# Optimization experiments

Measured on AMD Instinct MI355X. Metric: run time of the kernel, lower is better.

Reference implementation:

```python
import jax, jax.numpy as jnp
import numpy as np

B, Q, C = 16, 2048, 256
SCORE_THRESH = 0.05   # lowered from 0.7 so the mask is non-trivial with 256 classes
NMS_THRESH = 0.7
LABEL_OFFSET = 1e5    # batched_nms trick: offset boxes per class so cross-class IoU ~ 0


def box_cxcywh_to_xyxy(b):
    cx, cy, w, h = jnp.split(b, 4, axis=-1)
    return jnp.concatenate([cx - 0.5 * w, cy - 0.5 * h, cx + 0.5 * w, cy + 0.5 * h], axis=-1)


def pairwise_iou(boxes):
    # boxes: [N,4] xyxy -> iou: [N,N]
    area = jnp.clip(boxes[:, 2] - boxes[:, 0], 0) * jnp.clip(boxes[:, 3] - boxes[:, 1], 0)
    lt = jnp.maximum(boxes[:, None, :2], boxes[None, :, :2])
    rb = jnp.minimum(boxes[:, None, 2:], boxes[None, :, 2:])
    wh = jnp.clip(rb - lt, 0)
    inter = wh[..., 0] * wh[..., 1]
    union = area[:, None] + area[None, :] - inter
    return inter / jnp.maximum(union, 1e-6)


def nms_single(boxes, scores, labels, valid):
    # Emulates torchvision batched_nms with fixed-size (padded) output:
    # returns score-sorted boxes/scores/labels plus a boolean keep mask.
    n = boxes.shape[0]
    boxes_off = boxes + labels.astype(boxes.dtype)[:, None] * LABEL_OFFSET
    order = jnp.argsort(jnp.where(valid, scores, -jnp.inf))[::-1]
    b_off = boxes_off[order]
    s = scores[order]
    l = labels[order]
    v = valid[order]
    iou = pairwise_iou(b_off)  # [N,N], class-offset so only same-class overlap
    idx = jnp.arange(n)

    def step(keep, x):
        row, i = x  # row: iou of box i vs all
        sup = (row > NMS_THRESH) & (idx > i) & keep[i]
        return keep & ~sup, None

    keep, _ = jax.lax.scan(step, v, (iou, idx))
    return boxes[order], s, l, keep & v


def setup_inputs() -> dict:
    key = jax.random.key(0)
    k1, k2, k3 = jax.random.split(key, 3)
    pred_logits = jax.random.normal(k1, (B, Q, C), dtype=jnp.float32)
    pred_boxes = jax.random.uniform(k2, (B, Q, 4), dtype=jnp.float32)
    target_sizes = jax.random.randint(k3, (B, 2), 480, 1333, dtype=jnp.int32)
    return {"pred_logits": pred_logits, "pred_boxes": pred_boxes, "target_sizes": target_sizes}


def reference(pred_logits, pred_boxes, target_sizes):
    prob = jax.nn.softmax(pred_logits, axis=-1)
    cls_prob = prob[..., :-1]            # drop 'no-object' class
    scores = cls_prob.max(axis=-1)       # [B,Q]
    labels = cls_prob.argmax(axis=-1)    # [B,Q]
    boxes = box_cxcywh_to_xyxy(pred_boxes)
    ts = target_sizes.astype(boxes.dtype)
    img_h, img_w = ts[:, 0], ts[:, 1]
    scale = jnp.stack([img_w, img_h, img_w, img_h], axis=1)  # [B,4]
    boxes = boxes * scale[:, None, :]
    valid = scores >= SCORE_THRESH
    out_boxes, out_scores, out_labels, keep = jax.vmap(nms_single)(boxes, scores, labels, valid)
    return out_boxes, out_scores, out_labels, keep
```

## Files before the change

### kernel.cpp

```cpp
#include <hip/hip_runtime.h>
#include <math.h>

#define NB 16
#define BQ 2048
#define NC 256
#define NL 255

typedef unsigned long long u64;
typedef unsigned int u32;
typedef unsigned short u16;
typedef unsigned char u8;

__device__ __forceinline__ u32 ord_f32(float f) {
  u32 b = __float_as_uint(f);
  return (b & 0x80000000u) ? ~b : (b | 0x80000000u);
}

__global__ __launch_bounds__(256) void score_box_kernel(
    const float* __restrict__ logits,
    const float* __restrict__ pboxes,
    const int* __restrict__ tsz,
    float* __restrict__ ws)
{
#pragma clang fp contract(off)
  const int lane = threadIdx.x & 63;
  const int g = lane & 15;
  const int wv = threadIdx.x >> 6;
  const int q = (blockIdx.x * 4 + wv) * 4 + (lane >> 4);
  const float* row = logits + (size_t)q * NC + g * 16;
  const float4 la = *reinterpret_cast<const float4*>(row);
  const float4 lb4 = *reinterpret_cast<const float4*>(row + 4);
  const float4 lc = *reinterpret_cast<const float4*>(row + 8);
  const float4 ld = *reinterpret_cast<const float4*>(row + 12);

  float m = fmaxf(fmaxf(fmaxf(la.x, la.y), fmaxf(la.z, la.w)),
           fmaxf(fmaxf(fmaxf(lb4.x, lb4.y), fmaxf(lb4.z, lb4.w)),
           fmaxf(fmaxf(fmaxf(lc.x, lc.y), fmaxf(lc.z, lc.w)),
                 fmaxf(fmaxf(ld.x, ld.y), fmaxf(ld.z, ld.w)))));
  #pragma unroll
  for (int d = 1; d < 16; d <<= 1) m = fmaxf(m, __shfl_xor(m, d));

  float4 ea, eb, ec, ed;
  ea.x = expf(la.x - m);  ea.y = expf(la.y - m);  ea.z = expf(la.z - m);  ea.w = expf(la.w - m);
  eb.x = expf(lb4.x - m); eb.y = expf(lb4.y - m); eb.z = expf(lb4.z - m); eb.w = expf(lb4.w - m);
  ec.x = expf(lc.x - m);  ec.y = expf(lc.y - m);  ec.z = expf(lc.z - m);  ec.w = expf(lc.w - m);
  ed.x = expf(ld.x - m);  ed.y = expf(ld.y - m);  ed.z = expf(ld.z - m);  ed.w = expf(ld.w - m);

  float s = (((ea.x + ea.y) + (ea.z + ea.w)) + ((eb.x + eb.y) + (eb.z + eb.w)))
          + (((ec.x + ec.y) + (ec.z + ec.w)) + ((ed.x + ed.y) + (ed.z + ed.w)));
  #pragma unroll
  for (int d = 1; d < 16; d <<= 1) s += __shfl_xor(s, d);

  const int c0 = g * 16;
  float bp = ea.x / s; int bc = c0;
  float p;
  p = ea.y / s; if (p > bp) { bp = p; bc = c0 + 1; }
  p = ea.z / s; if (p > bp) { bp = p; bc = c0 + 2; }
  p = ea.w / s; if (p > bp) { bp = p; bc = c0 + 3; }
  p = eb.x / s; if (p > bp) { bp = p; bc = c0 + 4; }
  p = eb.y / s; if (p > bp) { bp = p; bc = c0 + 5; }
  p = eb.z / s; if (p > bp) { bp = p; bc = c0 + 6; }
  p = eb.w / s; if (p > bp) { bp = p; bc = c0 + 7; }
  p = ec.x / s; if (p > bp) { bp = p; bc = c0 + 8; }
  p = ec.y / s; if (p > bp) { bp = p; bc = c0 + 9; }
  p = ec.z / s; if (p > bp) { bp = p; bc = c0 + 10; }
  p = ec.w / s; if (p > bp) { bp = p; bc = c0 + 11; }
  p = ed.x / s; if (p > bp) { bp = p; bc = c0 + 12; }
  p = ed.y / s; if (p > bp) { bp = p; bc = c0 + 13; }
  p = ed.z / s; if (p > bp) { bp = p; bc = c0 + 14; }
  p = ed.w / s; if (g != 15 && p > bp) { bp = p; bc = c0 + 15; }
  #pragma unroll
  for (int d = 1; d < 16; d <<= 1) {
    const float op = __shfl_xor(bp, d);
    const int   oc = __shfl_xor(bc, d);
    if (op > bp || (op == bp && oc < bc)) { bp = op; bc = oc; }
  }

  if (g == 0) {
    const int b = q >> 11;
    float hf = (float)tsz[b * 2 + 0];
    float wf = (float)tsz[b * 2 + 1];
    float4 pb = *reinterpret_cast<const float4*>(pboxes + (size_t)q * 4);
    float hw = 0.5f * pb.z, hh = 0.5f * pb.w;
    float4 ob;
    ob.x = (pb.x - hw) * wf;
    ob.y = (pb.y - hh) * hf;
    ob.z = (pb.x + hw) * wf;
    ob.w = (pb.y + hh) * hf;
    *reinterpret_cast<float4*>(ws + (size_t)q * 4) = ob;
    ws[NB * BQ * 4 + q] = bp;
    ws[NB * BQ * 5 + q] = (float)bc;
  }
}

__global__ __launch_bounds__(1024) void sort_nms_kernel(
    const float* __restrict__ ws, float* __restrict__ out)
{
#pragma clang fp contract(off)
  __shared__ __align__(16) u64 cvk[BQ];
  __shared__ u32 rnk[BQ];
  __shared__ u32 lgl[BQ];
  __shared__ float4 bxo[BQ];
  __shared__ u32 stg_g[BQ];
  __shared__ u16 gpos[BQ];
  __shared__ u8 grpk[BQ];
  __shared__ u32 offl[256];
  __shared__ u32 kcnt[256];
  __shared__ u32 wval[16], winv[16];

  const int b = blockIdx.x;
  const int tid = threadIdx.x;
  const int lane = tid & 63;
  const int wv = tid >> 6;
  const float* bws = ws + (size_t)b * BQ * 4;
  const float* sws = ws + NB * BQ * 4 + (size_t)b * BQ;
  const float* lws = ws + NB * BQ * 5 + (size_t)b * BQ;
  float* boxes_g  = out + (size_t)b * BQ * 4;
  float* scores_g = out + NB * BQ * 4 + (size_t)b * BQ;
  float* labels_g = out + NB * BQ * 5 + (size_t)b * BQ;
  float* keep_g   = out + NB * BQ * 6 + (size_t)b * BQ;

  const int q0 = 2 * tid;
  float2 s2 = *reinterpret_cast<const float2*>(sws + q0);
  float2 lf = *reinterpret_cast<const float2*>(lws + q0);
  float4 bb0 = *reinterpret_cast<const float4*>(bws + (size_t)q0 * 4);
  float4 bb1 = *reinterpret_cast<const float4*>(bws + (size_t)q0 * 4 + 4);
  const u32 l0 = (u32)(int)lf.x, l1 = (u32)(int)lf.y;
  rnk[tid] = 0; rnk[tid + 1024] = 0;
  lgl[tid] = 0; lgl[tid + 1024] = 0;
  if (tid < 256) kcnt[tid] = 0;
  const bool v0 = (s2.x >= 0.05f), v1 = (s2.y >= 0.05f);
  const u64 f0 = ((u64)ord_f32(s2.x) << 32) | ((u32)q0 << 8) | l0;
  const u64 f1 = ((u64)ord_f32(s2.y) << 32) | ((u32)(q0 + 1) << 8) | l1;
  const u64 b0 = __ballot(v0), b1 = __ballot(v1);
  if (lane == 0) {
    const u32 c = (u32)(__popcll(b0) + __popcll(b1));
    wval[wv] = c;
    winv[wv] = 128u - c;
  }
  __syncthreads();

  int nv = 0, voff = 0, ioff = 0;
  #pragma unroll
  for (int w = 0; w < 16; ++w) {
    const int c = (int)wval[w];
    nv += c;
    if (w < wv) { voff += c; ioff += (int)winv[w]; }
  }
  const int tinv = BQ - nv;
  const u64 below = (1ull << lane) - 1ull;
  const int vr0 = voff + (int)__popcll(b0 & below) + (int)__popcll(b1 & below);
  const int ir0 = ioff + (int)__popcll(~b0 & below) + (int)__popcll(~b1 & below);
  const int vr1 = vr0 + (v0 ? 1 : 0);
  const int ir1 = ir0 + (v0 ? 0 : 1);
  if (v0) cvk[vr0] = f0;
  else {
    const int ip = nv + (tinv - 1 - ir0);
    *reinterpret_cast<float4*>(boxes_g + (size_t)ip * 4) = bb0;
    scores_g[ip] = s2.x; labels_g[ip] = lf.x; keep_g[ip] = 0.0f;
  }
  if (v1) cvk[vr1] = f1;
  else {
    const int ip = nv + (tinv - 1 - ir1);
    *reinterpret_cast<float4*>(boxes_g + (size_t)ip * 4) = bb1;
    scores_g[ip] = s2.y; labels_g[ip] = lf.y; keep_g[ip] = 0.0f;
  }
  __syncthreads();

  const int nvc = (nv + 63) >> 6;
  {
    const int nitems = nvc * nvc;
    for (int it = wv; it < nitems; it += 16) {
      const int sc_ = it / nvc;
      const int jc = it - sc_ * nvc;
      const int slot = (sc_ << 6) + lane;
      const u64 ki = cvk[slot];
      const u32 li = (u32)ki & 255u;
      const int j0 = jc << 6;
      int lim = nv - j0; if (lim > 64) lim = 64;
      const u64* jp = &cvk[j0];
      u32 cgt = 0, lgt = 0, llt = 0;
      #pragma unroll 8
      for (int l = 0; l < lim; ++l) {
        const u64 kj = jp[l];
        const u32 lj = (u32)kj & 255u;
        const u32 gx = (kj > ki) ? 1u : 0u;
        cgt += gx;
        lgt += gx & ((lj == li) ? 1u : 0u);
        llt += (lj < li) ? 1u : 0u;
      }
      if (slot < nv) {
        if (cgt) atomicAdd(&rnk[slot], cgt);
        if (lgt | llt) atomicAdd(&lgl[slot], (lgt << 16) | llt);
      }
    }
  }
  __syncthreads();

  for (int slot = tid; slot < nv; slot += 1024) {
    const u64 ki = cvk[slot];
    const u32 p = rnk[slot];
    const u32 ll = lgl[slot];
    const u32 lgt = ll >> 16, llt = ll & 0xFFFFu;
    const u32 oi = (u32)(ki >> 8) & (BQ - 1);
    const u32 li = (u32)ki & 255u;
    const float4 A = *reinterpret_cast<const float4*>(bws + (size_t)oi * 4);
    *reinterpret_cast<float4*>(boxes_g + (size_t)p * 4) = A;
    scores_g[p] = __uint_as_float((u32)(ki >> 32) & 0x7FFFFFFFu);
    labels_g[p] = (float)li;
    const float lc = (float)li * 100000.0f;
    float4 Ao;
    Ao.x = A.x + lc; Ao.y = A.y + lc; Ao.z = A.z + lc; Ao.w = A.w + lc;
    bxo[p] = Ao;
    gpos[llt + lgt] = (u16)p;
    stg_g[p] = (llt << 16) | lgt;
    offl[li] = llt;
    atomicAdd(&kcnt[li], 1u);
  }
  __syncthreads();

  for (int p = tid; p < nv; p += 1024) {
    const u32 sg = stg_g[p];
    const u32 st = sg >> 16, g = sg & 0xFFFFu;
    if (g < 64) {
      const float4 Ao = bxo[p];
      const float areaA = fmaxf(Ao.z - Ao.x, 0.0f) * fmaxf(Ao.w - Ao.y, 0.0f);
      u64 m = 0;
      for (u32 r = 0; r < g; ++r) {
        const int p2 = gpos[st + r];
        const float4 Bo = bxo[p2];
        const float areaB = fmaxf(Bo.z - Bo.x, 0.0f) * fmaxf(Bo.w - Bo.y, 0.0f);
        const float ltx = fmaxf(Ao.x, Bo.x), lty = fmaxf(Ao.y, Bo.y);
        const float rbx = fminf(Ao.z, Bo.z), rby = fminf(Ao.w, Bo.w);
        const float iw = fmaxf(rbx - ltx, 0.0f), ih = fmaxf(rby - lty, 0.0f);
        const float inter = iw * ih;
        const float uni = (areaA + areaB) - inter;
        const float iou = inter / fmaxf(uni, 1e-6f);
        if (iou > 0.7f) m |= (1ull << r);
      }
      cvk[st + g] = m;
    }
  }
  __syncthreads();

  if (tid < NL) {
    const int k = (int)kcnt[tid];
    if (k > 0) {
      const int st = (int)offl[tid];
      if (k <= 64) {
        u64 kept = 0;
        for (int r = 0; r < k; ++r) {
          const u64 m = cvk[st + r];
          const int keep = ((m & kept) == 0) ? 1 : 0;
          kept |= (u64)keep << r;
          keep_g[gpos[st + r]] = keep ? 1.0f : 0.0f;
        }
      } else {
        for (int a = 0; a < k; ++a) {
          const int p = gpos[st + a];
          const float4 Ao = bxo[p];
          const float areaA = fmaxf(Ao.z - Ao.x, 0.0f) * fmaxf(Ao.w - Ao.y, 0.0f);
          int keep = 1;
          for (int e = 0; e < a; ++e) {
            if (!grpk[st + e]) continue;
            const int p2 = gpos[st + e];
            const float4 Bo = bxo[p2];
            const float areaB = fmaxf(Bo.z - Bo.x, 0.0f) * fmaxf(Bo.w - Bo.y, 0.0f);
            const float ltx = fmaxf(Ao.x, Bo.x), lty = fmaxf(Ao.y, Bo.y);
            const float rbx = fminf(Ao.z, Bo.z), rby = fminf(Ao.w, Bo.w);
            const float iw = fmaxf(rbx - ltx, 0.0f), ih = fmaxf(rby - lty, 0.0f);
            const float inter = iw * ih;
            const float uni = (areaA + areaB) - inter;
            const float iou = inter / fmaxf(uni, 1e-6f);
            if (iou > 0.7f) { keep = 0; break; }
          }
          grpk[st + a] = (u8)keep;
          keep_g[p] = keep ? 1.0f : 0.0f;
        }
      }
    }
  }
}

extern "C" void kernel_launch(void* const* d_in, const int* in_sizes, int n_in,
                              void* d_out, int out_size, void* d_ws, size_t ws_size,
                              hipStream_t stream) {
  const float* logits = (const float*)d_in[0];
  const float* pboxes = (const float*)d_in[1];
  const int*   tsz    = (const int*)d_in[2];
  float* out = (float*)d_out;
  float* ws  = (float*)d_ws;
  score_box_kernel<<<NB * BQ / 16, 256, 0, stream>>>(logits, pboxes, tsz, ws);
  sort_nms_kernel<<<NB, 1024, 0, stream>>>(ws, out);
}
```

Measured before the change: 36.85 us.

## Register-block rank counting, cache boxes in LDS, stage intermediates in output buffer

The all-pairs rank/label-count loop now gives each lane two query keys and reads the key array with 128-bit shared loads. The tail is padded with a sentinel key so the inner loop has a fixed trip count of 64 and no per-iteration bound check. Boxes are staged in shared memory so the scatter after ranking reads from LDS instead of global memory. The score kernel now writes its intermediates straight into the output buffer, which the sort kernel reads and then overwrites in place, so the separate workspace is no longer used. The cost is about 32 KB more LDS per block and a dependence on every read finishing before the first in-place write.

```diff
diff --git a/kernel.cpp b/kernel.cpp
--- a/kernel.cpp
+++ b/kernel.cpp
@@ -20,7 +20,7 @@
     const float* __restrict__ logits,
     const float* __restrict__ pboxes,
     const int* __restrict__ tsz,
-    float* __restrict__ ws)
+    float* __restrict__ out)
 {
 #pragma clang fp contract(off)
   const int lane = threadIdx.x & 63;
@@ -87,19 +87,19 @@
     ob.y = (pb.y - hh) * hf;
     ob.z = (pb.x + hw) * wf;
     ob.w = (pb.y + hh) * hf;
-    *reinterpret_cast<float4*>(ws + (size_t)q * 4) = ob;
-    ws[NB * BQ * 4 + q] = bp;
-    ws[NB * BQ * 5 + q] = (float)bc;
+    *reinterpret_cast<float4*>(out + (size_t)q * 4) = ob;
+    out[NB * BQ * 4 + q] = bp;
+    out[NB * BQ * 5 + q] = (float)bc;
   }
 }
 
-__global__ __launch_bounds__(1024) void sort_nms_kernel(
-    const float* __restrict__ ws, float* __restrict__ out)
+__global__ __launch_bounds__(1024) void sort_nms_kernel(float* __restrict__ out)
 {
 #pragma clang fp contract(off)
   __shared__ __align__(16) u64 cvk[BQ];
   __shared__ u32 rnk[BQ];
   __shared__ u32 lgl[BQ];
+  __shared__ float4 bx[BQ];
   __shared__ float4 bxo[BQ];
   __shared__ u32 stg_g[BQ];
   __shared__ u16 gpos[BQ];
@@ -112,20 +112,18 @@
   const int tid = threadIdx.x;
   const int lane = tid & 63;
   const int wv = tid >> 6;
-  const float* bws = ws + (size_t)b * BQ * 4;
-  const float* sws = ws + NB * BQ * 4 + (size_t)b * BQ;
-  const float* lws = ws + NB * BQ * 5 + (size_t)b * BQ;
   float* boxes_g  = out + (size_t)b * BQ * 4;
   float* scores_g = out + NB * BQ * 4 + (size_t)b * BQ;
   float* labels_g = out + NB * BQ * 5 + (size_t)b * BQ;
   float* keep_g   = out + NB * BQ * 6 + (size_t)b * BQ;
 
   const int q0 = 2 * tid;
-  float2 s2 = *reinterpret_cast<const float2*>(sws + q0);
-  float2 lf = *reinterpret_cast<const float2*>(lws + q0);
-  float4 bb0 = *reinterpret_cast<const float4*>(bws + (size_t)q0 * 4);
-  float4 bb1 = *reinterpret_cast<const float4*>(bws + (size_t)q0 * 4 + 4);
+  float2 s2 = *reinterpret_cast<const float2*>(scores_g + q0);
+  float2 lf = *reinterpret_cast<const float2*>(labels_g + q0);
+  float4 bb0 = *reinterpret_cast<const float4*>(boxes_g + (size_t)q0 * 4);
+  float4 bb1 = *reinterpret_cast<const float4*>(boxes_g + (size_t)q0 * 4 + 4);
   const u32 l0 = (u32)(int)lf.x, l1 = (u32)(int)lf.y;
+  bx[q0] = bb0; bx[q0 + 1] = bb1;
   rnk[tid] = 0; rnk[tid + 1024] = 0;
   lgl[tid] = 0; lgl[tid + 1024] = 0;
   if (tid < 256) kcnt[tid] = 0;
@@ -165,33 +163,42 @@
     *reinterpret_cast<float4*>(boxes_g + (size_t)ip * 4) = bb1;
     scores_g[ip] = s2.y; labels_g[ip] = lf.y; keep_g[ip] = 0.0f;
   }
-  __syncthreads();
-
   const int nvc = (nv + 63) >> 6;
+  for (int pp = nv + tid; pp < (nvc << 6); pp += 1024) cvk[pp] = 0xFFull;
+  __syncthreads();
+
   {
-    const int nitems = nvc * nvc;
+    const int nvS = (nv + 127) >> 7;
+    const int nitems = nvS * nvc;
     for (int it = wv; it < nitems; it += 16) {
       const int sc_ = it / nvc;
       const int jc = it - sc_ * nvc;
-      const int slot = (sc_ << 6) + lane;
-      const u64 ki = cvk[slot];
-      const u32 li = (u32)ki & 255u;
-      const int j0 = jc << 6;
-      int lim = nv - j0; if (lim > 64) lim = 64;
-      const u64* jp = &cvk[j0];
-      u32 cgt = 0, lgt = 0, llt = 0;
-      #pragma unroll 8
-      for (int l = 0; l < lim; ++l) {
-        const u64 kj = jp[l];
-        const u32 lj = (u32)kj & 255u;
-        const u32 gx = (kj > ki) ? 1u : 0u;
-        cgt += gx;
-        lgt += gx & ((lj == li) ? 1u : 0u);
-        llt += (lj < li) ? 1u : 0u;
-      }
-      if (slot < nv) {
-        if (cgt) atomicAdd(&rnk[slot], cgt);
-        if (lgt | llt) atomicAdd(&lgl[slot], (lgt << 16) | llt);
+      const int sb = (sc_ << 7) + lane;
+      const u64 ki0 = cvk[sb];
+      const u64 ki1 = cvk[sb + 64];
+      const u32 li0 = (u32)ki0 & 255u, li1 = (u32)ki1 & 255u;
+      const ulonglong2* jp2 = reinterpret_cast<const ulonglong2*>(&cvk[jc << 6]);
+      u32 c0 = 0, c1 = 0, g0 = 0, g1 = 0, t0 = 0, t1 = 0;
+      #pragma unroll 4
+      for (int l2 = 0; l2 < 32; ++l2) {
+        const ulonglong2 kj = jp2[l2];
+        const u32 ljx = (u32)kj.x & 255u, ljy = (u32)kj.y & 255u;
+        const u32 gx0 = (kj.x > ki0) ? 1u : 0u, gy0 = (kj.y > ki0) ? 1u : 0u;
+        const u32 gx1 = (kj.x > ki1) ? 1u : 0u, gy1 = (kj.y > ki1) ? 1u : 0u;
+        c0 += gx0 + gy0;
+        c1 += gx1 + gy1;
+        g0 += (gx0 & ((ljx == li0) ? 1u : 0u)) + (gy0 & ((ljy == li0) ? 1u : 0u));
+        g1 += (gx1 & ((ljx == li1) ? 1u : 0u)) + (gy1 & ((ljy == li1) ? 1u : 0u));
+        t0 += ((ljx < li0) ? 1u : 0u) + ((ljy < li0) ? 1u : 0u);
+        t1 += ((ljx < li1) ? 1u : 0u) + ((ljy < li1) ? 1u : 0u);
+      }
+      if (sb < nv) {
+        if (c0) atomicAdd(&rnk[sb], c0);
+        if (g0 | t0) atomicAdd(&lgl[sb], (g0 << 16) | t0);
+      }
+      if (sb + 64 < nv) {
+        if (c1) atomicAdd(&rnk[sb + 64], c1);
+        if (g1 | t1) atomicAdd(&lgl[sb + 64], (g1 << 16) | t1);
       }
     }
   }
@@ -204,7 +211,7 @@
     const u32 lgt = ll >> 16, llt = ll & 0xFFFFu;
     const u32 oi = (u32)(ki >> 8) & (BQ - 1);
     const u32 li = (u32)ki & 255u;
-    const float4 A = *reinterpret_cast<const float4*>(bws + (size_t)oi * 4);
+    const float4 A = bx[oi];
     *reinterpret_cast<float4*>(boxes_g + (size_t)p * 4) = A;
     scores_g[p] = __uint_as_float((u32)(ki >> 32) & 0x7FFFFFFFu);
     labels_g[p] = (float)li;
@@ -289,7 +296,6 @@
   const float* pboxes = (const float*)d_in[1];
   const int*   tsz    = (const int*)d_in[2];
   float* out = (float*)d_out;
-  float* ws  = (float*)d_ws;
-  score_box_kernel<<<NB * BQ / 16, 256, 0, stream>>>(logits, pboxes, tsz, ws);
-  sort_nms_kernel<<<NB, 1024, 0, stream>>>(ws, out);
+  score_box_kernel<<<NB * BQ / 16, 256, 0, stream>>>(logits, pboxes, tsz, out);
+  sort_nms_kernel<<<NB, 1024, 0, stream>>>(out);
 }
```

After: 39.20 us. 1.06x slower.
